# Kernel optimization log

Hardware: AMD Instinct MI355X
Metric: run time of the kernel (lower is better)

Reference implementation:

```python
import jax, jax.numpy as jnp
import numpy as np

B, S, D, H = 2, 2048, 1024, 16
DK = D // H  # 64


def setup_inputs() -> dict:
    key = jax.random.key(0)
    ks = jax.random.split(key, 10)
    query = jax.random.normal(ks[0], (B, S, D), dtype=jnp.float32)
    key_t = jax.random.normal(ks[1], (B, S, D), dtype=jnp.float32)
    value = jax.random.normal(ks[2], (B, S, D), dtype=jnp.float32)
    # binary mask [batch, q_size, k_size]: causal lower-triangular, same per batch
    mask = jnp.broadcast_to(jnp.tril(jnp.ones((S, S), dtype=jnp.float32)), (B, S, S))
    sc = 0.02
    Wq = jax.random.normal(ks[3], (D, D), dtype=jnp.float32) * sc
    bq = jnp.zeros((D,), dtype=jnp.float32)
    Wk = jax.random.normal(ks[4], (D, D), dtype=jnp.float32) * sc
    bk = jnp.zeros((D,), dtype=jnp.float32)
    Wv = jax.random.normal(ks[5], (D, D), dtype=jnp.float32) * sc
    bv = jnp.zeros((D,), dtype=jnp.float32)
    return {"query": query, "key": key_t, "value": value, "mask": mask,
            "Wq": Wq, "bq": bq, "Wk": Wk, "bk": bk, "Wv": Wv, "bv": bv}


def reference(query, key, value, mask, Wq, bq, Wk, bk, Wv, bv):
    # ReLU-activated Q/K/V projections (Dense(..., activation='relu'))
    Q = jax.nn.relu(query @ Wq + bq)   # [B, Sq, D]
    K = jax.nn.relu(key @ Wk + bk)     # [B, Sk, D]
    V = jax.nn.relu(value @ Wv + bv)   # [B, Sk, D]
    b, sq, _ = Q.shape
    sk = K.shape[1]
    # split-concat head trick == reshape last dim into (H, DK) heads
    Qh = Q.reshape(b, sq, H, DK)
    Kh = K.reshape(b, sk, H, DK)
    Vh = V.reshape(b, sk, H, DK)
    scores = jnp.einsum('bqhd,bkhd->bhqk', Qh, Kh) / jnp.sqrt(jnp.float32(DK))
    m = mask[:, None, :, :]  # broadcast over heads (mask_expander tiles over h)
    scores = scores * m + (1.0 - m) * (-1e10)
    attn = jax.nn.softmax(scores, axis=-1)  # dropout is a no-op (see notes)
    out = jnp.einsum('bhqk,bkhd->bqhd', attn, Vh).reshape(b, sq, H * DK)
    return out
```

## Files before the change

kernel.cpp:

```cpp
#include <hip/hip_runtime.h>
#include <hip/hip_bf16.h>

#define B_  2
#define S_  2048
#define D_  1024
#define H_  16
#define DK_ 64
#define NR  (B_*S_)
#define QT_ 16
#define CPP 20

typedef __bf16 bf16_t;
typedef __attribute__((ext_vector_type(8)))  __bf16 bf16x8;
typedef __attribute__((ext_vector_type(4)))  float  f32x4;
typedef __attribute__((ext_vector_type(16))) float  f32x16;

#define QSCALE (0.125f * 1.44269504088896340736f)

__device__ inline void gl_lds16(const void* g, void* l) {
  __builtin_amdgcn_global_load_lds(
      (const __attribute__((address_space(1))) void*)g,
      (__attribute__((address_space(3))) void*)l, 16, 0, 0);
}

__device__ inline unsigned pack2(float a, float b) {
  union { bf16_t h[2]; unsigned u; } x;
  x.h[0] = (bf16_t)a; x.h[1] = (bf16_t)b;
  return x.u;
}

__device__ inline float fast_exp2(float x) {
  float r;
  asm("v_exp_f32 %0, %1" : "=v"(r) : "v"(x));
  return r;
}

__device__ inline bf16x8 frag(const bf16_t* p, int r, int j) {
  return *(const bf16x8*)(p + r * 64 + ((j ^ (r & 7)) * 8));
}
__device__ inline bf16x8 frag32(const bf16_t* p, int r, int j) {
  return *(const bf16x8*)(p + r * 32 + ((j ^ ((r >> 1) & 3)) * 8));
}

__device__ const unsigned char ord_p[CPP] = {7,6,5,4,3,2,7,6,5,4,7,6,1,7,5,3,6,4,2,0};
__device__ const unsigned char ord_c[CPP] = {0,0,0,0,0,0,1,1,1,1,2,2,0,3,2,1,3,2,1,0};
__device__ const unsigned char cbase[8]   = {0,1,2,4,6,9,12,16};

__global__ void cvt_fp32_bf16(const float* __restrict__ xq, const float* __restrict__ xk,
                              const float* __restrict__ xv,
                              bf16_t* __restrict__ yq, bf16_t* __restrict__ yk,
                              bf16_t* __restrict__ yv) {
  const int z = blockIdx.y;
  const float* x = z == 0 ? xq : z == 1 ? xk : xv;
  bf16_t*      y = z == 0 ? yq : z == 1 ? yk : yv;
  size_t i = ((size_t)blockIdx.x * 256 + threadIdx.x) * 8;
  float4 a = *(const float4*)(x + i);
  float4 b = *(const float4*)(x + i + 4);
  union { bf16_t h[8]; uint4 u; } o;
  o.h[0] = (bf16_t)a.x; o.h[1] = (bf16_t)a.y; o.h[2] = (bf16_t)a.z; o.h[3] = (bf16_t)a.w;
  o.h[4] = (bf16_t)b.x; o.h[5] = (bf16_t)b.y; o.h[6] = (bf16_t)b.z; o.h[7] = (bf16_t)b.w;
  *(uint4*)(y + i) = o.u;
}

__global__ void transpose_cvt(const float* __restrict__ wq, const float* __restrict__ wk,
                              const float* __restrict__ wv,
                              bf16_t* __restrict__ oq, bf16_t* __restrict__ ok,
                              bf16_t* __restrict__ ov) {
  const int z = blockIdx.z;
  const float* W = z == 0 ? wq : z == 1 ? wk : wv;
  bf16_t*     WT = z == 0 ? oq : z == 1 ? ok : ov;
  __shared__ float t[32][33];
  int x  = blockIdx.x * 32 + threadIdx.x;
  int y0 = blockIdx.y * 32;
  for (int i = threadIdx.y; i < 32; i += 8)
    t[i][threadIdx.x] = W[(size_t)(y0 + i) * D_ + x];
  __syncthreads();
  int k  = y0 + threadIdx.x;
  int n0 = blockIdx.x * 32;
  for (int i = threadIdx.y; i < 32; i += 8)
    WT[(size_t)(n0 + i) * D_ + k] = (bf16_t)t[threadIdx.x][i];
}

__global__ __launch_bounds__(256, 3) void gemm_qkv(
    const bf16_t* __restrict__ Xq, const bf16_t* __restrict__ Xk, const bf16_t* __restrict__ Xv,
    const bf16_t* __restrict__ Wq, const bf16_t* __restrict__ Wk, const bf16_t* __restrict__ Wv,
    const float* __restrict__ bq, const float* __restrict__ bk, const float* __restrict__ bv,
    bf16_t* __restrict__ Yq, bf16_t* __restrict__ Yk, bf16_t* __restrict__ Yv)
{
  const int z = blockIdx.z;
  const bf16_t* X    = z == 0 ? Xq : z == 1 ? Xk : Xv;
  const bf16_t* WT   = z == 0 ? Wq : z == 1 ? Wk : Wv;
  const float*  bias = z == 0 ? bq : z == 1 ? bk : bv;
  bf16_t*       Y    = z == 0 ? Yq : z == 1 ? Yk : Yv;
  const float scale  = z == 0 ? QSCALE : 1.0f;
  const int transposedV = (z == 2);

  __shared__ bf16_t As[3][128 * 32];
  __shared__ bf16_t Bs[3][128 * 32];
  const int m0 = blockIdx.x * 128, n0 = blockIdx.y * 128;
  const int t = threadIdx.x, l = t & 63, w = t >> 6;
  const int wm = (w & 1) * 64, wn = (w >> 1) * 64;
  const int lr = l & 15, lg4 = l >> 4;

  f32x4 acc[4][4] = {};

  auto stage = [&](int bi, int k0) {
    #pragma unroll
    for (int i = 0; i < 2; i++) {
      int c = i * 256 + t;
      int row = c >> 2, j0c = c & 3;
      int sc = (j0c ^ ((row >> 1) & 3)) * 8;
      gl_lds16(X  + (size_t)(m0 + row) * D_ + k0 + sc, &As[bi][c * 8]);
      gl_lds16(WT + (size_t)(n0 + row) * D_ + k0 + sc, &Bs[bi][c * 8]);
    }
  };

  stage(0, 0);
  stage(1, 32);
  asm volatile("s_waitcnt vmcnt(4)" ::: "memory");
  __builtin_amdgcn_s_barrier();
  __builtin_amdgcn_sched_barrier(0);

  const int NSTEP = D_ / 32;
  for (int p = 0; p < NSTEP; ++p) {
    const int cur = p - (p / 3) * 3;

    if (p + 2 < NSTEP) {
      const int nb = (p + 2) - ((p + 2) / 3) * 3;
      stage(nb, (p + 2) * 32);
    }

    bf16x8 af[4], bfr[4];
    #pragma unroll
    for (int mf = 0; mf < 4; mf++)
      af[mf] = frag32(&As[cur][0], wm + mf * 16 + lr, lg4);
    #pragma unroll
    for (int nf = 0; nf < 4; nf++)
      bfr[nf] = frag32(&Bs[cur][0], wn + nf * 16 + lr, lg4);
    __builtin_amdgcn_s_setprio(1);
    #pragma unroll
    for (int mf = 0; mf < 4; mf++)
      #pragma unroll
      for (int nf = 0; nf < 4; nf++)
        acc[mf][nf] = __builtin_amdgcn_mfma_f32_16x16x32_bf16(
            af[mf], bfr[nf], acc[mf][nf], 0, 0, 0);
    __builtin_amdgcn_s_setprio(0);

    if (p + 1 < NSTEP) {
      if (p + 2 < NSTEP) asm volatile("s_waitcnt vmcnt(4)" ::: "memory");
      else               asm volatile("s_waitcnt vmcnt(0)" ::: "memory");
      __builtin_amdgcn_s_barrier();
      __builtin_amdgcn_sched_barrier(0);
    }
  }

  #pragma unroll
  for (int nf = 0; nf < 4; nf++) {
    int col = n0 + wn + nf * 16 + lr;
    float bvv = bias[col];
    #pragma unroll
    for (int mf = 0; mf < 4; mf++) {
      if (!transposedV) {
        #pragma unroll
        for (int r = 0; r < 4; r++) {
          int row = m0 + wm + mf * 16 + lg4 * 4 + r;
          float v = fmaxf(acc[mf][nf][r] + bvv, 0.f) * scale;
          Y[(size_t)row * D_ + col] = (bf16_t)v;
        }
      } else {
        int row0 = m0 + wm + mf * 16 + lg4 * 4;
        int bb = row0 >> 11, s0 = row0 & (S_ - 1);
        int hh = col >> 6,  dk = col & (DK_ - 1);
        union { bf16_t h[4]; unsigned long long u; } pk;
        #pragma unroll
        for (int r = 0; r < 4; r++)
          pk.h[r] = (bf16_t)fmaxf(acc[mf][nf][r] + bvv, 0.f);
        *(unsigned long long*)&Y[(((size_t)(bb * H_ + hh)) * DK_ + dk) * S_ + s0] = pk.u;
      }
    }
  }
}

__device__ inline void qkt(const bf16_t* kl, const bf16x8* qf, int lq, int hh,
                           f32x16& s0, f32x16& s1) {
  #pragma unroll
  for (int s = 0; s < 4; s++) {
    bf16x8 k0 = frag(kl, lq, 2 * s + hh);
    bf16x8 k1 = frag(kl, lq + 32, 2 * s + hh);
    s0 = __builtin_amdgcn_mfma_f32_32x32x16_bf16(k0, qf[s], s0, 0, 0, 0);
    s1 = __builtin_amdgcn_mfma_f32_32x32x16_bf16(k1, qf[s], s1, 0, 0, 0);
  }
}

__device__ inline void cmask(f32x16& s0, f32x16& s1, int kb, int q, int hh) {
  #pragma unroll
  for (int r = 0; r < 16; r++) {
    int krow = kb + (r & 3) + 8 * (r >> 2) + 4 * hh;
    if (krow > q)      s0[r] = -1e30f;
    if (krow + 32 > q) s1[r] = -1e30f;
  }
}

__device__ inline void pv_quad(const f32x16& p0, const f32x16& p1,
                               const bf16_t* vl, int lq, int hh,
                               f32x16& o0, f32x16& o1) {
  #pragma unroll
  for (int st = 0; st < 4; st++) {
    const f32x16& ps = (st < 2) ? p0 : p1;
    const int bb = (st & 1) * 8;
    unsigned lo0 = pack2(ps[bb + 0], ps[bb + 1]), lo1 = pack2(ps[bb + 2], ps[bb + 3]);
    unsigned hi0 = pack2(ps[bb + 4], ps[bb + 5]), hi1 = pack2(ps[bb + 6], ps[bb + 7]);
    unsigned sA = hh ? lo0 : hi0, sB = hh ? lo1 : hi1;
    unsigned rA = __shfl_xor(sA, 32, 64), rB = __shfl_xor(sB, 32, 64);
    union { unsigned u[4]; bf16x8 v; } pf;
    pf.u[0] = hh ? rA : lo0;  pf.u[1] = hh ? rB : lo1;
    pf.u[2] = hh ? hi0 : rA;  pf.u[3] = hh ? hi1 : rB;
    bf16x8 v0 = frag(vl, lq, 2 * st + hh);
    bf16x8 v1 = frag(vl, lq + 32, 2 * st + hh);
    o0 = __builtin_amdgcn_mfma_f32_32x32x16_bf16(v0, pf.v, o0, 0, 0, 0);
    o1 = __builtin_amdgcn_mfma_f32_32x32x16_bf16(v1, pf.v, o1, 0, 0, 0);
  }
}

__global__ __launch_bounds__(512, 4) void attn_fwd(
    const bf16_t* __restrict__ Q, const bf16_t* __restrict__ K,
    const bf16_t* __restrict__ VT, bf16_t* __restrict__ PO,
    float* __restrict__ PL)
{
  __shared__ bf16_t lbuf[3][8192];

  const int bx = blockIdx.x;
  const int unit = bx >> 5, bh = bx & 31;
  const int p_ = ord_p[unit], ch = ord_c[unit];
  const int b = bh >> 4, h = bh & 15;
  const int kt0 = ch * 8;
  const int nt = min(8, (4 * p_ + 4) - kt0);
  const int slotbase = (bh * CPP + cbase[p_] + ch) * 2;

  const int t = threadIdx.x, w = t >> 6, l = t & 63;
  const int u = w >> 2, w4 = w & 3;
  const int qt = 2 * p_ + u;
  const int q0 = qt * 128 + w4 * 32;
  const int lq = l & 31, hh = l >> 5;
  const int qq = q0 + lq;
  const int nfull = 2 * qt + (w4 >> 1);

  const bf16_t* Qb = Q  + ((size_t)(b * S_ + qq)) * D_ + h * DK_;
  const bf16_t* Kb = K  + ((size_t)b * S_) * D_ + h * DK_;
  const bf16_t* Vb = VT + ((size_t)(b * H_ + h)) * ((size_t)DK_ * S_);

  const int r0 = t >> 3, j0 = t & 7;
  const int jx = (j0 ^ (r0 & 7)) * 8;

  #define STAGE_TILE(bi, kt_) do {                                    \
    const int kb_ = (kt_) << 6;                                       \
    bf16_t* Lb = lbuf[bi];                                            \
    gl_lds16(Kb + (size_t)(kb_ + r0) * D_ + jx, Lb + t * 8);          \
    gl_lds16(Vb + (size_t)r0 * S_ + kb_ + jx,   Lb + 4096 + t * 8);   \
  } while (0)

  bf16x8 qf[4];
  #pragma unroll
  for (int s = 0; s < 4; s++)
    qf[s] = *(const bf16x8*)(Qb + s * 16 + hh * 8);
  asm volatile("s_waitcnt vmcnt(0)" ::: "memory");
  #pragma unroll
  for (int s = 0; s < 4; s++)
    asm volatile("" : "+v"(qf[s]));

  f32x16 o0 = {}, o1 = {};
  f32x16 lacc = {};

  STAGE_TILE(0, kt0);
  STAGE_TILE(1, kt0 + 1);
  asm volatile("s_waitcnt vmcnt(2)" ::: "memory");
  __builtin_amdgcn_s_barrier();
  __builtin_amdgcn_sched_barrier(0);

  for (int p = 0; p < nt; ++p) {
    const int kt = kt0 + p;
    const int cur = p - (p / 3) * 3;

    if (p + 2 < nt) {
      const int nb = (p + 2) - ((p + 2) / 3) * 3;
      STAGE_TILE(nb, kt + 2);
    }

    if (kt <= nfull) {
      const bf16_t* kl = lbuf[cur];
      const bf16_t* vl = lbuf[cur] + 4096;

      f32x16 s0 = {}, s1 = {};
      __builtin_amdgcn_s_setprio(1);
      qkt(kl, qf, lq, hh, s0, s1);
      __builtin_amdgcn_s_setprio(0);
      if (kt == nfull) cmask(s0, s1, kt << 6, qq, hh);

      f32x16 p0, p1;
      #pragma unroll
      for (int r2 = 0; r2 < 16; r2++) {
        p0[r2] = fast_exp2(s0[r2]);
        p1[r2] = fast_exp2(s1[r2]);
        lacc[r2] += p0[r2] + p1[r2];
      }

      __builtin_amdgcn_s_setprio(1);
      pv_quad(p0, p1, vl, lq, hh, o0, o1);
      __builtin_amdgcn_s_setprio(0);
    }

    if (p + 1 < nt) {
      if (p + 2 < nt) asm volatile("s_waitcnt vmcnt(2)" ::: "memory");
      else            asm volatile("s_waitcnt vmcnt(0)" ::: "memory");
      __builtin_amdgcn_s_barrier();
      __builtin_amdgcn_sched_barrier(0);
    }
  }
  #undef STAGE_TILE

  float lrun = 0.f;
  #pragma unroll
  for (int r2 = 0; r2 < 16; r2++) lrun += lacc[r2];
  lrun += __shfl_xor(lrun, 32, 64);

  bf16_t* po = PO + (size_t)(slotbase + u) * 8192;
  #pragma unroll
  for (int r2 = 0; r2 < 16; r2++) {
    int dk = (r2 & 3) + 8 * (r2 >> 2) + 4 * hh;
    po[dk * 128 + w4 * 32 + lq]        = (bf16_t)o0[r2];
    po[(dk + 32) * 128 + w4 * 32 + lq] = (bf16_t)o1[r2];
  }
  if (hh == 0)
    PL[(size_t)(slotbase + u) * 128 + w4 * 32 + lq] = lrun;
}

__global__ __launch_bounds__(256, 4) void attn_combine(
    const bf16_t* __restrict__ PO, const float* __restrict__ PL,
    float* __restrict__ out)
{
  const int bx = blockIdx.x;
  const int b = bx >> 8, h = (bx >> 4) & 15, qt = bx & 15;
  const int bh = b * H_ + h;
  const int p_ = qt >> 1, u = qt & 1;
  const int nc = (p_ >> 1) + 1;
  const int slot0 = (bh * CPP + cbase[p_]) * 2 + u;

  __shared__ float ls[64][132];
  __shared__ float inv[128];

  const int t = threadIdx.x;

  float acc[4][8];
  #pragma unroll
  for (int i = 0; i < 4; i++)
    #pragma unroll
    for (int j = 0; j < 8; j++) acc[i][j] = 0.f;

  for (int c = 0; c < nc; ++c) {
    const bf16_t* po = PO + (size_t)(slot0 + 2 * c) * 8192;
    #pragma unroll
    for (int i = 0; i < 4; i++) {
      bf16x8 v = *(const bf16x8*)(po + i * 2048 + t * 8);
      #pragma unroll
      for (int j = 0; j < 8; j++) acc[i][j] += (float)v[j];
    }
  }

  if (t < 128) {
    float s = 0.f;
    for (int c = 0; c < nc; ++c) s += PL[(size_t)(slot0 + 2 * c) * 128 + t];
    inv[t] = 1.0f / s;
  }

  #pragma unroll
  for (int i = 0; i < 4; i++)
    #pragma unroll
    for (int j = 0; j < 8; j++)
      ls[(t >> 4) + 16 * i][(t & 15) * 8 + j] = acc[i][j];
  __syncthreads();

  const int q = t >> 1, c0 = (t & 1) * 32;
  const float iv = inv[q];
  float* op = out + ((size_t)(b * S_ + qt * 128 + q)) * D_ + h * DK_ + c0;
  #pragma unroll
  for (int v = 0; v < 8; v++) {
    float4 x = { ls[c0 + 4 * v][q] * iv,     ls[c0 + 4 * v + 1][q] * iv,
                 ls[c0 + 4 * v + 2][q] * iv, ls[c0 + 4 * v + 3][q] * iv };
    *(float4*)(op + 4 * v) = x;
  }
}

extern "C" void kernel_launch(void* const* d_in, const int* in_sizes, int n_in,
                              void* d_out, int out_size, void* d_ws, size_t ws_size,
                              hipStream_t stream) {
  const float* query = (const float*)d_in[0];
  const float* keyi  = (const float*)d_in[1];
  const float* val   = (const float*)d_in[2];
  const float* Wq = (const float*)d_in[4];
  const float* bq = (const float*)d_in[5];
  const float* Wk = (const float*)d_in[6];
  const float* bk = (const float*)d_in[7];
  const float* Wv = (const float*)d_in[8];
  const float* bv = (const float*)d_in[9];
  float* out = (float*)d_out;

  const size_t XB = (size_t)NR * D_;
  const size_t WB = (size_t)D_ * D_;
  bf16_t* ws  = (bf16_t*)d_ws;
  bf16_t* Xq  = ws;
  bf16_t* Xk  = Xq  + XB;
  bf16_t* Xv  = Xk  + XB;
  bf16_t* WTq = Xv  + XB;
  bf16_t* WTk = WTq + WB;
  bf16_t* WTv = WTk + WB;
  bf16_t* Qm  = WTv + WB;
  bf16_t* Km  = Qm  + XB;
  bf16_t* VTm = Km  + XB;
  bf16_t* PO  = ws;
  float*  PL  = (float*)((char*)d_ws + 22u * 1024 * 1024);

  dim3 cgrid(XB / (256 * 8), 3);
  cvt_fp32_bf16<<<cgrid, 256, 0, stream>>>(query, keyi, val, Xq, Xk, Xv);

  dim3 tgrid(D_ / 32, D_ / 32, 3), tblk(32, 8);
  transpose_cvt<<<tgrid, tblk, 0, stream>>>(Wq, Wk, Wv, WTq, WTk, WTv);

  dim3 ggrid(NR / 128, D_ / 128, 3);
  gemm_qkv<<<ggrid, 256, 0, stream>>>(Xq, Xk, Xv, WTq, WTk, WTv,
                                      bq, bk, bv, Qm, Km, VTm);

  attn_fwd<<<dim3(32 * CPP), 512, 0, stream>>>(Qm, Km, VTm, PO, PL);
  attn_combine<<<dim3(B_ * H_ * QT_), 256, 0, stream>>>(PO, PL, out);
}
```

Baseline: 102.1 us.

## Fuse fp32-to-bf16 activation conversion into QKV GEMM A-tile loading

Drops the separate conversion kernel. The GEMM now loads fp32 activations into registers one stage ahead, converts them to bf16 and writes them into swizzled LDS, while weights still use direct global-to-LDS loads. This removes a full launch plus a round trip of the bf16 activation copy through memory. In exchange the GEMM reads twice the bytes for A, holds more registers, and the wait counts are adjusted by hand, which could hurt occupancy or pipelining.

```diff
diff --git a/kernel.cpp b/kernel.cpp
--- a/kernel.cpp
+++ b/kernel.cpp
@@ -45,22 +45,6 @@
 __device__ const unsigned char ord_p[CPP] = {7,6,5,4,3,2,7,6,5,4,7,6,1,7,5,3,6,4,2,0};
 __device__ const unsigned char ord_c[CPP] = {0,0,0,0,0,0,1,1,1,1,2,2,0,3,2,1,3,2,1,0};
 __device__ const unsigned char cbase[8]   = {0,1,2,4,6,9,12,16};
-
-__global__ void cvt_fp32_bf16(const float* __restrict__ xq, const float* __restrict__ xk,
-                              const float* __restrict__ xv,
-                              bf16_t* __restrict__ yq, bf16_t* __restrict__ yk,
-                              bf16_t* __restrict__ yv) {
-  const int z = blockIdx.y;
-  const float* x = z == 0 ? xq : z == 1 ? xk : xv;
-  bf16_t*      y = z == 0 ? yq : z == 1 ? yk : yv;
-  size_t i = ((size_t)blockIdx.x * 256 + threadIdx.x) * 8;
-  float4 a = *(const float4*)(x + i);
-  float4 b = *(const float4*)(x + i + 4);
-  union { bf16_t h[8]; uint4 u; } o;
-  o.h[0] = (bf16_t)a.x; o.h[1] = (bf16_t)a.y; o.h[2] = (bf16_t)a.z; o.h[3] = (bf16_t)a.w;
-  o.h[4] = (bf16_t)b.x; o.h[5] = (bf16_t)b.y; o.h[6] = (bf16_t)b.z; o.h[7] = (bf16_t)b.w;
-  *(uint4*)(y + i) = o.u;
-}
 
 __global__ void transpose_cvt(const float* __restrict__ wq, const float* __restrict__ wk,
                               const float* __restrict__ wv,
@@ -81,14 +65,16 @@
     WT[(size_t)(n0 + i) * D_ + k] = (bf16_t)t[threadIdx.x][i];
 }
 
+struct AReg { float4 a[4]; };
+
 __global__ __launch_bounds__(256, 3) void gemm_qkv(
-    const bf16_t* __restrict__ Xq, const bf16_t* __restrict__ Xk, const bf16_t* __restrict__ Xv,
+    const float* __restrict__ XFq, const float* __restrict__ XFk, const float* __restrict__ XFv,
     const bf16_t* __restrict__ Wq, const bf16_t* __restrict__ Wk, const bf16_t* __restrict__ Wv,
     const float* __restrict__ bq, const float* __restrict__ bk, const float* __restrict__ bv,
     bf16_t* __restrict__ Yq, bf16_t* __restrict__ Yk, bf16_t* __restrict__ Yv)
 {
   const int z = blockIdx.z;
-  const bf16_t* X    = z == 0 ? Xq : z == 1 ? Xk : Xv;
+  const float*  XF   = z == 0 ? XFq : z == 1 ? XFk : XFv;
   const bf16_t* WT   = z == 0 ? Wq : z == 1 ? Wk : Wv;
   const float*  bias = z == 0 ? bq : z == 1 ? bk : bv;
   bf16_t*       Y    = z == 0 ? Yq : z == 1 ? Yk : Yv;
@@ -104,20 +90,48 @@
 
   f32x4 acc[4][4] = {};
 
-  auto stage = [&](int bi, int k0) {
+  auto loadA = [&](int k0) {
+    AReg r;
     #pragma unroll
     for (int i = 0; i < 2; i++) {
       int c = i * 256 + t;
-      int row = c >> 2, j0c = c & 3;
-      int sc = (j0c ^ ((row >> 1) & 3)) * 8;
-      gl_lds16(X  + (size_t)(m0 + row) * D_ + k0 + sc, &As[bi][c * 8]);
+      int row = c >> 2, j = c & 3;
+      const float* src = XF + (size_t)(m0 + row) * D_ + k0 + j * 8;
+      r.a[2 * i]     = *(const float4*)src;
+      r.a[2 * i + 1] = *(const float4*)(src + 4);
+    }
+    return r;
+  };
+  auto cvtWriteA = [&](int bi, const AReg& r) {
+    #pragma unroll
+    for (int i = 0; i < 2; i++) {
+      int c = i * 256 + t;
+      int row = c >> 2, j = c & 3;
+      union { bf16_t h[8]; bf16x8 v; } pk;
+      #pragma unroll
+      for (int k = 0; k < 4; k++) {
+        pk.h[k]     = (bf16_t)r.a[2 * i][k];
+        pk.h[4 + k] = (bf16_t)r.a[2 * i + 1][k];
+      }
+      *(bf16x8*)&As[bi][row * 32 + ((j ^ ((row >> 1) & 3)) * 8)] = pk.v;
+    }
+  };
+  auto stageB = [&](int bi, int k0) {
+    #pragma unroll
+    for (int i = 0; i < 2; i++) {
+      int c = i * 256 + t;
+      int row = c >> 2, j = c & 3;
+      int sc = (j ^ ((row >> 1) & 3)) * 8;
       gl_lds16(WT + (size_t)(n0 + row) * D_ + k0 + sc, &Bs[bi][c * 8]);
     }
   };
 
-  stage(0, 0);
-  stage(1, 32);
-  asm volatile("s_waitcnt vmcnt(4)" ::: "memory");
+  AReg aA = loadA(0);
+  stageB(0, 0);
+  AReg aNext = loadA(32);
+  stageB(1, 32);
+  cvtWriteA(0, aA);
+  asm volatile("s_waitcnt vmcnt(6) lgkmcnt(0)" ::: "memory");
   __builtin_amdgcn_s_barrier();
   __builtin_amdgcn_sched_barrier(0);
 
@@ -125,9 +139,12 @@
   for (int p = 0; p < NSTEP; ++p) {
     const int cur = p - (p / 3) * 3;
 
-    if (p + 2 < NSTEP) {
+    AReg aNew;
+    const bool more = (p + 2 < NSTEP);
+    if (more) {
       const int nb = (p + 2) - ((p + 2) / 3) * 3;
-      stage(nb, (p + 2) * 32);
+      aNew = loadA((p + 2) * 32);
+      stageB(nb, (p + 2) * 32);
     }
 
     bf16x8 af[4], bfr[4];
@@ -147,10 +164,13 @@
     __builtin_amdgcn_s_setprio(0);
 
     if (p + 1 < NSTEP) {
-      if (p + 2 < NSTEP) asm volatile("s_waitcnt vmcnt(4)" ::: "memory");
-      else               asm volatile("s_waitcnt vmcnt(0)" ::: "memory");
+      const int nb1 = (p + 1) - ((p + 1) / 3) * 3;
+      cvtWriteA(nb1, aNext);
+      if (more) asm volatile("s_waitcnt vmcnt(6) lgkmcnt(0)" ::: "memory");
+      else      asm volatile("s_waitcnt vmcnt(0) lgkmcnt(0)" ::: "memory");
       __builtin_amdgcn_s_barrier();
       __builtin_amdgcn_sched_barrier(0);
+      aNext = aNew;
     }
   }
 
@@ -407,10 +427,7 @@
   const size_t XB = (size_t)NR * D_;
   const size_t WB = (size_t)D_ * D_;
   bf16_t* ws  = (bf16_t*)d_ws;
-  bf16_t* Xq  = ws;
-  bf16_t* Xk  = Xq  + XB;
-  bf16_t* Xv  = Xk  + XB;
-  bf16_t* WTq = Xv  + XB;
+  bf16_t* WTq = ws + 3 * XB;
   bf16_t* WTk = WTq + WB;
   bf16_t* WTv = WTk + WB;
   bf16_t* Qm  = WTv + WB;
@@ -419,14 +436,11 @@
   bf16_t* PO  = ws;
   float*  PL  = (float*)((char*)d_ws + 22u * 1024 * 1024);
 
-  dim3 cgrid(XB / (256 * 8), 3);
-  cvt_fp32_bf16<<<cgrid, 256, 0, stream>>>(query, keyi, val, Xq, Xk, Xv);
-
   dim3 tgrid(D_ / 32, D_ / 32, 3), tblk(32, 8);
   transpose_cvt<<<tgrid, tblk, 0, stream>>>(Wq, Wk, Wv, WTq, WTk, WTv);
 
   dim3 ggrid(NR / 128, D_ / 128, 3);
-  gemm_qkv<<<ggrid, 256, 0, stream>>>(Xq, Xk, Xv, WTq, WTk, WTv,
+  gemm_qkv<<<ggrid, 256, 0, stream>>>(query, keyi, val, WTq, WTk, WTv,
                                       bq, bk, bv, Qm, Km, VTm);
 
   attn_fwd<<<dim3(32 * CPP), 512, 0, stream>>>(Qm, Km, VTm, PO, PL);
```

Result: faster. 95.88 us (-6.1%).
